# Performance work log

Hardware: AMD Instinct MI355X
Metric: run time of the kernel (lower is better)

The kernel has to match this reference:

```python
import jax, jax.numpy as jnp
import numpy as np

N, E, F, H, G, EPS = 50000, 500000, 128, 192, 256, 1e-5


def setup_inputs() -> dict:
    key = jax.random.key(0)
    ks = jax.random.split(key, 16)
    s = 0.05
    return {
        "x": jax.random.normal(ks[0], (N, F), jnp.float32),
        "edge_index": jax.random.randint(ks[1], (2, E), 0, N),
        "batch": jnp.sort(jax.random.randint(ks[2], (N,), 0, G)),
        "num_graphs": G,
        "w_rel0": jax.random.normal(ks[3], (H, F)) * s,
        "b_rel0": jnp.zeros((H,), jnp.float32),
        "w_root0": jax.random.normal(ks[4], (H, F)) * s,
        "w_rel": jax.random.normal(ks[5], (3, H, H)) * s,
        "b_rel": jnp.zeros((3, H), jnp.float32),
        "w_root": jax.random.normal(ks[6], (3, H, H)) * s,
        "bn_gamma": jnp.ones((4, H), jnp.float32),
        "bn_beta": jnp.zeros((4, H), jnp.float32),
        "head_w1": jax.random.normal(ks[7], (H, H)) * s,
        "head_b1": jnp.zeros((H,), jnp.float32),
        "head_w2": jax.random.normal(ks[8], (H, H)) * s,
        "head_b2": jnp.zeros((H,), jnp.float32),
        "out_w": jax.random.normal(ks[9], (1, H)) * s,
        "out_b": jnpp if False else jnp.zeros((1,), jnp.float32),
    }


def _conv_bn_relu(x, src, dst, n_nodes, wr, br, wroot, gamma, beta):
    # PyG GraphConv: out_i = lin_rel(sum_{j->i} x_j) + lin_root(x_i)
    agg = jax.ops.segment_sum(x[src], dst, num_segments=n_nodes)  # [N, d]
    h = agg @ wr.T + br + x @ wroot.T                             # [N, H]
    mu = h.mean(axis=0)
    var = h.var(axis=0)  # biased, as torch BN train mode
    h = (h - mu) * jax.lax.rsqrt(var + EPS) * gamma + beta
    return jax.nn.relu(h)


def reference(x, edge_index, batch, num_graphs, w_rel0, b_rel0, w_root0,
              w_rel, b_rel, w_root, bn_gamma, bn_beta,
              head_w1, head_b1, head_w2, head_b2, out_w, out_b):
    src, dst = edge_index[0], edge_index[1]
    n_nodes = x.shape[0]
    h = _conv_bn_relu(x, src, dst, n_nodes, w_rel0, b_rel0, w_root0,
                      bn_gamma[0], bn_beta[0])
    for i in range(3):
        h = _conv_bn_relu(h, src, dst, n_nodes, w_rel[i], b_rel[i], w_root[i],
                          bn_gamma[i + 1], bn_beta[i + 1])
    # global mean pool per graph
    sums = jax.ops.segment_sum(h, batch, num_segments=num_graphs)   # [G, H]
    cnts = jax.ops.segment_sum(jnp.ones((n_nodes,), h.dtype), batch,
                               num_segments=num_graphs)
    g = sums / jnp.maximum(cnts, 1.0)[:, None]
    # MLP head (dropout = eval) + output linear
    hh = jax.nn.relu(g @ head_w1.T + head_b1) @ head_w2.T + head_b2
    out = hh @ out_w.T + out_b                                      # [G, 1]
    return out[:, 0]
```

## Files before the change

kernel.cpp:

```cpp
#include <hip/hip_runtime.h>

#define HD 192
#define FD0 128
#define NG 256
#define BNEPS 1e-5f

#define STAT_S  1048576.0f
#define STAT_IS (1.0f / 1048576.0f)
#define POOL_S  65536.0f
#define POOL_IS (1.0f / 65536.0f)

typedef unsigned short u16;
typedef __attribute__((ext_vector_type(8))) short bf16x8;
typedef __attribute__((ext_vector_type(4))) float f32x4;

static inline int idiv(int a, int b) { return (a + b - 1) / b; }

__device__ __forceinline__ float b2f(u16 u) {
    unsigned int v = ((unsigned int)u) << 16;
    return __builtin_bit_cast(float, v);
}
__device__ __forceinline__ float b2f_lo(unsigned int u) {
    return __builtin_bit_cast(float, u << 16);
}
__device__ __forceinline__ float b2f_hi(unsigned int u) {
    return __builtin_bit_cast(float, u & 0xffff0000u);
}
__device__ __forceinline__ u16 f2b(float f) {
    unsigned int x = __builtin_bit_cast(unsigned int, f);
    return (u16)((x + 0x7FFFu + ((x >> 16) & 1u)) >> 16);
}

__device__ __forceinline__ void async_cp16(const void* g, void* l) {
    __builtin_amdgcn_global_load_lds(
        (const __attribute__((address_space(1))) unsigned int*)g,
        (__attribute__((address_space(3))) unsigned int*)l, 16, 0, 0);
}

__global__ __launch_bounds__(256) void convert_bf16(const float* __restrict__ in,
                                                    u16* __restrict__ out, int n4)
{
    const int i = blockIdx.x * 256 + threadIdx.x;
    if (i >= n4) return;
    const float4 v = ((const float4*)in)[i];
    u16 o[4] = { f2b(v.x), f2b(v.y), f2b(v.z), f2b(v.w) };
    ((ushort4*)out)[i] = *(ushort4*)o;
}

__device__ __forceinline__ void pack_one(const float* __restrict__ wr,
    const float* __restrict__ wt, u16* __restrict__ out, int K, int idx)
{
    const int j  = idx & 7;
    const int t  = idx >> 3;
    const int c  = t & 15;
    const int kg = (t >> 4) & 3;
    const int rest = t >> 6;
    const int fglob = rest % 12;
    const int chunk = rest / 12;
    const int col = fglob * 16 + c;
    const int k   = chunk * 32 + kg * 8 + j;
    const float v = (k < K) ? wr[(size_t)col * K + k] : wt[(size_t)col * K + (k - K)];
    out[idx] = f2b(v);
}

__global__ __launch_bounds__(256) void pack_fuse(const float* __restrict__ wr0,
    const float* __restrict__ wt0, const float* __restrict__ w_rel,
    const float* __restrict__ w_root, const float* __restrict__ hw1,
    const float* __restrict__ hw2, u16* __restrict__ wp0,
    u16* __restrict__ wp123, float* __restrict__ w1t, float* __restrict__ w2t)
{
    const int T0 = HD * 2 * FD0;
    const int T1 = HD * 2 * HD;
    const int TW = HD * HD;
    int idx = blockIdx.x * 256 + threadIdx.x;
    if (idx < T0) { pack_one(wr0, wt0, wp0, FD0, idx); return; }
    idx -= T0;
    if (idx < 3 * T1) {
        const int li = idx / T1;
        const int r  = idx - li * T1;
        pack_one(w_rel + (size_t)li * HD * HD, w_root + (size_t)li * HD * HD,
                 wp123 + (size_t)li * T1, HD, r);
        return;
    }
    idx -= 3 * T1;
    if (idx >= 2 * TW) return;
    const float* w = (idx < TW) ? hw1 : hw2;
    float*       o = (idx < TW) ? w1t : w2t;
    const int r = (idx < TW) ? idx : idx - TW;
    const int t = r % HD, k = r / HD;
    o[r] = w[(size_t)t * HD + k];
}

__global__ __launch_bounds__(256) void hist_kernel(const int* __restrict__ dst,
                                                   int* __restrict__ deg, int E)
{
    const int e = blockIdx.x * 256 + threadIdx.x;
    if (e < E) atomicAdd(&deg[dst[e]], 1);
}

__global__ __launch_bounds__(256) void scan_partial(const int* __restrict__ deg,
                                                    int* __restrict__ psum, int N)
{
    __shared__ int s[256];
    const int t = threadIdx.x;
    const int i = blockIdx.x * 256 + t;
    s[t] = (i < N) ? deg[i] : 0;
    __syncthreads();
    for (int off = 128; off > 0; off >>= 1) {
        if (t < off) s[t] += s[t + off];
        __syncthreads();
    }
    if (t == 0) psum[blockIdx.x] = s[0];
}

__global__ __launch_bounds__(256) void scan_small(int* __restrict__ psum, int M)
{
    __shared__ int s[256];
    const int t = threadIdx.x;
    s[t] = (t < M) ? psum[t] : 0;
    __syncthreads();
    for (int off = 1; off < 256; off <<= 1) {
        const int u = (t >= off) ? s[t - off] : 0;
        __syncthreads();
        s[t] += u;
        __syncthreads();
    }
    if (t < M) psum[t] = (t == 0) ? 0 : s[t - 1];
}

__global__ __launch_bounds__(256) void scan_expand(int* __restrict__ deg,
    const int* __restrict__ psum, int* __restrict__ rowptr, int N, int E)
{
    __shared__ int s[256];
    const int t = threadIdx.x;
    const int i = blockIdx.x * 256 + t;
    const int v = (i < N) ? deg[i] : 0;
    s[t] = v;
    __syncthreads();
    for (int off = 1; off < 256; off <<= 1) {
        const int u = (t >= off) ? s[t - off] : 0;
        __syncthreads();
        s[t] += u;
        __syncthreads();
    }
    if (i < N) {
        const int base = psum[blockIdx.x] + s[t] - v;
        rowptr[i] = base;
        deg[i]    = base;
    }
    if (i == N - 1) rowptr[N] = E;
}

__global__ __launch_bounds__(256) void fill_kernel(const int* __restrict__ src,
    const int* __restrict__ dst, int* __restrict__ cursor,
    int* __restrict__ eidx, int E)
{
    const int e = blockIdx.x * 256 + threadIdx.x;
    if (e >= E) return;
    const int p = atomicAdd(&cursor[dst[e]], 1);
    eidx[p] = src[e];
}

template<int FD>
__global__ __launch_bounds__(256) void gather_kernel(
    const u16* __restrict__ hb, const int* __restrict__ rowptr,
    const int* __restrict__ eidx, u16* __restrict__ aggb, int N)
{
    constexpr int GW = FD / 32;
    constexpr int ND = GW / 2;
    const int lane = threadIdx.x & 63;
    const int half = lane >> 5;
    const int g    = lane & 31;
    const int n    = blockIdx.x * 4 + (threadIdx.x >> 6);
    if (n >= N) return;
    const int beg = rowptr[n], end = rowptr[n + 1];

    float acc[GW];
#pragma unroll
    for (int i = 0; i < GW; ++i) acc[i] = 0.f;

    int j = beg + half;
    for (; j + 6 < end; j += 8) {
        const int s0 = eidx[j],     s1 = eidx[j + 2];
        const int s2 = eidx[j + 4], s3 = eidx[j + 6];
        const unsigned int* p0 = (const unsigned int*)(hb + (size_t)s0 * FD + g * GW);
        const unsigned int* p1 = (const unsigned int*)(hb + (size_t)s1 * FD + g * GW);
        const unsigned int* p2 = (const unsigned int*)(hb + (size_t)s2 * FD + g * GW);
        const unsigned int* p3 = (const unsigned int*)(hb + (size_t)s3 * FD + g * GW);
        unsigned int u0[ND], u1[ND], u2[ND], u3[ND];
#pragma unroll
        for (int d = 0; d < ND; ++d) { u0[d] = p0[d]; u1[d] = p1[d]; u2[d] = p2[d]; u3[d] = p3[d]; }
#pragma unroll
        for (int d = 0; d < ND; ++d) {
            acc[2*d]   += b2f_lo(u0[d]) + b2f_lo(u1[d]) + b2f_lo(u2[d]) + b2f_lo(u3[d]);
            acc[2*d+1] += b2f_hi(u0[d]) + b2f_hi(u1[d]) + b2f_hi(u2[d]) + b2f_hi(u3[d]);
        }
    }
    for (; j < end; j += 2) {
        const int s0 = eidx[j];
        const unsigned int* p0 = (const unsigned int*)(hb + (size_t)s0 * FD + g * GW);
#pragma unroll
        for (int d = 0; d < ND; ++d) {
            const unsigned int u = p0[d];
            acc[2*d]   += b2f_lo(u);
            acc[2*d+1] += b2f_hi(u);
        }
    }
#pragma unroll
    for (int i = 0; i < GW; ++i) acc[i] += __shfl_xor(acc[i], 32);

    if (half == 0) {
        unsigned int* q = (unsigned int*)(aggb + (size_t)n * FD + g * GW);
#pragma unroll
        for (int d = 0; d < ND; ++d) {
            const u16 lo = f2b(acc[2*d]);
            const u16 hi = f2b(acc[2*d+1]);
            q[d] = (unsigned int)lo | ((unsigned int)hi << 16);
        }
    }
}

template<int K1, int K2>
__global__ __launch_bounds__(512, 1) void gemm_mfma(
    const u16* __restrict__ A1, const u16* __restrict__ A2,
    const u16* __restrict__ Wb, const float* __restrict__ bias,
    u16* __restrict__ Hout, long long* __restrict__ statsq, int N)
{
    constexpr int KC  = K1 + K2;
    constexpr int NC  = KC / 32;
    constexpr int NC1 = K1 / 32;
    __shared__ u16 bsh[HD * KC];

    const int tid  = threadIdx.x;
    const int wave = tid >> 6, lane = tid & 63;
    const int c = lane & 15, kg = lane >> 4;
    const int row0 = blockIdx.x * 256 + wave * 32;

    {
        constexpr int NST = (HD * KC) / (512 * 8);
        const u16* wsrc = Wb + tid * 8;
        u16* ldst = bsh + tid * 8;
#pragma unroll
        for (int i = 0; i < NST; ++i)
            async_cp16(wsrc + i * 4096, ldst + i * 4096);
    }

    int arc[2];
#pragma unroll
    for (int m = 0; m < 2; ++m) {
        const int r = row0 + m * 16 + c;
        arc[m] = r < N ? r : N - 1;
    }

    f32x4 acc[2][12];
#pragma unroll
    for (int m = 0; m < 2; ++m)
#pragma unroll
        for (int f = 0; f < 12; ++f) acc[m][f] = (f32x4){0.f, 0.f, 0.f, 0.f};

    auto aload = [&](int ch, bf16x8* d) {
#pragma unroll
        for (int m = 0; m < 2; ++m) {
            const u16* p = (ch < NC1)
                ? (A1 + (size_t)arc[m] * K1 + ch * 32 + kg * 8)
                : (A2 + (size_t)arc[m] * K2 + (ch - NC1) * 32 + kg * 8);
            d[m] = *(const bf16x8*)p;
        }
    };

    bf16x8 a_cur[2], a_nxt[2];
    aload(0, a_cur);
    __syncthreads();

#pragma unroll
    for (int ch = 0; ch < NC; ++ch) {
        if (ch + 1 < NC) aload(ch + 1, a_nxt);
#pragma unroll
        for (int f = 0; f < 12; ++f) {
            const bf16x8 b = *(const bf16x8*)&bsh[ch * 6144 + f * 512 + kg * 128 + c * 8];
            acc[0][f] = __builtin_amdgcn_mfma_f32_16x16x32_bf16(a_cur[0], b, acc[0][f], 0, 0, 0);
            acc[1][f] = __builtin_amdgcn_mfma_f32_16x16x32_bf16(a_cur[1], b, acc[1][f], 0, 0, 0);
        }
        a_cur[0] = a_nxt[0]; a_cur[1] = a_nxt[1];
    }

    float s1v[12], s2v[12];
#pragma unroll
    for (int f = 0; f < 12; ++f) { s1v[f] = 0.f; s2v[f] = 0.f; }

#pragma unroll
    for (int f = 0; f < 12; ++f) {
        const int col = f * 16 + c;
        const float bv = bias[col];
#pragma unroll
        for (int m = 0; m < 2; ++m)
#pragma unroll
            for (int r = 0; r < 4; ++r) {
                const int orow = row0 + m * 16 + kg * 4 + r;
                if (orow < N) {
                    const float v = acc[m][f][r] + bv;
                    s1v[f] += v;
                    s2v[f] += v * v;
                    Hout[(size_t)orow * HD + col] = f2b(v);
                }
            }
    }
#pragma unroll
    for (int f = 0; f < 12; ++f) {
        s1v[f] += __shfl_xor(s1v[f], 16); s1v[f] += __shfl_xor(s1v[f], 32);
        s2v[f] += __shfl_xor(s2v[f], 16); s2v[f] += __shfl_xor(s2v[f], 32);
    }
    __syncthreads();
    float* red = (float*)bsh;
    if (kg == 0) {
#pragma unroll
        for (int f = 0; f < 12; ++f) {
            red[wave * HD + f * 16 + c]            = s1v[f];
            red[8 * HD + wave * HD + f * 16 + c]   = s2v[f];
        }
    }
    __syncthreads();
    if (tid < HD) {
        float a1 = 0.f, a2 = 0.f;
#pragma unroll
        for (int w = 0; w < 8; ++w) {
            a1 += red[w * HD + tid];
            a2 += red[8 * HD + w * HD + tid];
        }
        atomicAdd((unsigned long long*)&statsq[tid],
                  (unsigned long long)(long long)llrintf(a1 * STAT_S));
        atomicAdd((unsigned long long*)&statsq[HD + tid],
                  (unsigned long long)(long long)llrintf(a2 * STAT_S));
    }
}

__global__ __launch_bounds__(256) void norm_relu(const u16* __restrict__ hpre,
    u16* __restrict__ hb, const long long* __restrict__ statsq,
    const float* __restrict__ gamma, const float* __restrict__ beta, int N)
{
    __shared__ float sc[HD], sh[HD];
    const int t = threadIdx.x;
    if (t < HD) {
        const float inv = 1.0f / (float)N;
        const float sum = (float)statsq[t] * STAT_IS;
        const float sq  = (float)statsq[HD + t] * STAT_IS;
        const float mu  = sum * inv;
        const float var = sq * inv - mu * mu;
        const float s   = gamma[t] * rsqrtf(var + BNEPS);
        sc[t] = s; sh[t] = beta[t] - mu * s;
    }
    __syncthreads();
    const int idx = blockIdx.x * 256 + t;
    const int total = N * (HD / 8);
    if (idx >= total) return;
    const int c8 = idx % (HD / 8);
    uint4 packed = ((const uint4*)hpre)[idx];
    const u16* pu = (const u16*)&packed;
    u16 ob[8];
#pragma unroll
    for (int j = 0; j < 8; ++j) {
        const int cc = c8 * 8 + j;
        ob[j] = f2b(fmaxf(0.f, fmaf(b2f(pu[j]), sc[cc], sh[cc])));
    }
    ((uint4*)hb)[idx] = *(uint4*)ob;
}

__global__ __launch_bounds__(192) void pool_partial(const u16* __restrict__ hb,
    const int* __restrict__ batch, int* __restrict__ gsumq, int N)
{
    const int t   = threadIdx.x;
    const int rl  = t / 24;
    const int oct = t % 24;
    const int r0  = blockIdx.x * 256;
    const int rend = (r0 + 256 < N) ? r0 + 256 : N;

    float facc[8];
#pragma unroll
    for (int i = 0; i < 8; ++i) facc[i] = 0.f;
    int cur = -1;

    for (int r = r0 + rl; r < rend; r += 8) {
        const int b = batch[r];
        if (b != cur) {
            if (cur >= 0) {
                int* q = gsumq + (size_t)cur * HD + oct * 8;
#pragma unroll
                for (int i = 0; i < 8; ++i)
                    atomicAdd(&q[i], __float2int_rn(facc[i] * POOL_S));
            }
#pragma unroll
            for (int i = 0; i < 8; ++i) facc[i] = 0.f;
            cur = b;
        }
        const uint4 pv = *(const uint4*)(hb + (size_t)r * HD + oct * 8);
        const u16* pu = (const u16*)&pv;
#pragma unroll
        for (int i = 0; i < 8; ++i) facc[i] += b2f(pu[i]);
    }
    if (cur >= 0) {
        int* q = gsumq + (size_t)cur * HD + oct * 8;
#pragma unroll
        for (int i = 0; i < 8; ++i)
            atomicAdd(&q[i], __float2int_rn(facc[i] * POOL_S));
    }
}

__global__ __launch_bounds__(192) void head_kernel(
    const int* __restrict__ gsumq, const int* __restrict__ batch, int N,
    const float* __restrict__ w1t, const float* __restrict__ b1,
    const float* __restrict__ w2t, const float* __restrict__ b2,
    const float* __restrict__ ow, const float* __restrict__ ob,
    float* __restrict__ out)
{
    __shared__ float gv[HD];
    __shared__ float h1[HD];
    __shared__ float h2[HD];
    const int g = blockIdx.x;
    const int t = threadIdx.x;

    int lo = 0, hi = N;
    while (lo < hi) { int m = (lo + hi) >> 1; if (batch[m] < g) lo = m + 1; else hi = m; }
    const int start = lo;
    hi = N;
    while (lo < hi) { int m = (lo + hi) >> 1; if (batch[m] < g + 1) lo = m + 1; else hi = m; }
    const int end = lo;
    const float cnt = fmaxf((float)(end - start), 1.0f);

    gv[t] = (float)gsumq[(size_t)g * HD + t] * POOL_IS / cnt;
    __syncthreads();
    {
        float acc = b1[t];
#pragma unroll 4
        for (int k = 0; k < HD; ++k)
            acc = fmaf(gv[k], w1t[k * HD + t], acc);
        h1[t] = fmaxf(acc, 0.f);
    }
    __syncthreads();
    {
        float acc = b2[t];
#pragma unroll 4
        for (int k = 0; k < HD; ++k)
            acc = fmaf(h1[k], w2t[k * HD + t], acc);
        h2[t] = acc * ow[t];
    }
    __syncthreads();
    if (t < 64) {
        float s = h2[t] + h2[t + 64] + h2[t + 128];
#pragma unroll
        for (int d = 1; d < 64; d <<= 1) s += __shfl_xor(s, d);
        if (t == 0) out[g] = s + ob[0];
    }
}

extern "C" void kernel_launch(void* const* d_in, const int* in_sizes, int n_in,
                              void* d_out, int out_size, void* d_ws, size_t ws_size,
                              hipStream_t stream)
{
    const float* x       = (const float*)d_in[0];
    const int*   ei      = (const int*)d_in[1];
    const int*   batch   = (const int*)d_in[2];
    const float* w_rel0  = (const float*)d_in[4];
    const float* b_rel0  = (const float*)d_in[5];
    const float* w_root0 = (const float*)d_in[6];
    const float* w_rel   = (const float*)d_in[7];
    const float* b_rel   = (const float*)d_in[8];
    const float* w_root  = (const float*)d_in[9];
    const float* bn_g    = (const float*)d_in[10];
    const float* bn_b    = (const float*)d_in[11];
    const float* hw1     = (const float*)d_in[12];
    const float* hb1     = (const float*)d_in[13];
    const float* hw2     = (const float*)d_in[14];
    const float* hb2     = (const float*)d_in[15];
    const float* ow      = (const float*)d_in[16];
    const float* ob      = (const float*)d_in[17];
    float* out = (float*)d_out;

    const int N = in_sizes[0] / FD0;
    const int E = in_sizes[1] / 2;
    const int* src = ei;
    const int* dst = ei + E;
    const int M = idiv(N, 256);

    char* ws = (char*)d_ws;
    size_t off = 0;
    u16*   xb   = (u16*)(ws + off);   off += (size_t)N * FD0 * 2;
    u16*   hb   = (u16*)(ws + off);   off += (size_t)N * HD * 2;
    u16*   aggb = (u16*)(ws + off);   off += (size_t)N * HD * 2;
    u16*   hpre = (u16*)(ws + off);   off += (size_t)N * HD * 2;
    u16*   wp0  = (u16*)(ws + off);   off += (size_t)HD * 2 * FD0 * 2;
    u16*   wp123= (u16*)(ws + off);   off += (size_t)3 * HD * 2 * HD * 2;
    off = (off + 15) & ~(size_t)15;
    float* w1t = (float*)(ws + off); off += (size_t)HD * HD * 4;
    float* w2t = (float*)(ws + off); off += (size_t)HD * HD * 4;
    long long* statsq4 = (long long*)(ws + off); off += 4 * 2 * HD * sizeof(long long);
    int*   gsumq  = (int*)(ws + off); off += (size_t)NG * HD * 4;
    int*   rowptr = (int*)(ws + off); off += (size_t)(N + 1) * 4;
    int*   deg    = (int*)(ws + off); off += (size_t)N * 4;
    int*   psum   = (int*)(ws + off); off += (size_t)M * 4;
    int*   eidx   = (int*)(ws + off); off += (size_t)E * 4;

    const dim3 b256(256), b512(512), b192(192);

    convert_bf16<<<idiv(N * FD0 / 4, 256), b256, 0, stream>>>(x, xb, N * FD0 / 4);
    pack_fuse<<<idiv(HD * 2 * FD0 + 3 * HD * 2 * HD + 2 * HD * HD, 256), b256, 0,
                stream>>>(w_rel0, w_root0, w_rel, w_root, hw1, hw2,
                          wp0, wp123, w1t, w2t);
    hipMemsetAsync(statsq4, 0, 4 * 2 * HD * sizeof(long long) + (size_t)NG * HD * 4,
                   stream);
    hipMemsetAsync(deg, 0, (size_t)N * sizeof(int), stream);
    hist_kernel<<<idiv(E, 256), b256, 0, stream>>>(dst, deg, E);
    scan_partial<<<M, b256, 0, stream>>>(deg, psum, N);
    scan_small<<<1, b256, 0, stream>>>(psum, M);
    scan_expand<<<M, b256, 0, stream>>>(deg, psum, rowptr, N, E);
    fill_kernel<<<idiv(E, 256), b256, 0, stream>>>(src, dst, deg, eidx, E);

    gather_kernel<FD0><<<idiv(N, 4), b256, 0, stream>>>(xb, rowptr, eidx, aggb, N);
    gemm_mfma<FD0, FD0><<<idiv(N, 256), b512, 0, stream>>>(aggb, xb, wp0, b_rel0,
                                                           hpre, statsq4, N);
    norm_relu<<<idiv(N * (HD / 8), 256), b256, 0, stream>>>(hpre, hb, statsq4,
                                                            bn_g, bn_b, N);

    for (int i = 0; i < 3; ++i) {
        long long* statsq = statsq4 + (size_t)(i + 1) * 2 * HD;
        gather_kernel<HD><<<idiv(N, 4), b256, 0, stream>>>(hb, rowptr, eidx, aggb, N);
        gemm_mfma<HD, HD><<<idiv(N, 256), b512, 0, stream>>>(
            aggb, hb, wp123 + (size_t)i * HD * 2 * HD,
            b_rel + (size_t)i * HD, hpre, statsq, N);
        norm_relu<<<idiv(N * (HD / 8), 256), b256, 0, stream>>>(hpre, hb, statsq,
            bn_g + (size_t)(i + 1) * HD, bn_b + (size_t)(i + 1) * HD, N);
    }

    pool_partial<<<idiv(N, 256), b192, 0, stream>>>(hb, batch, gsumq, N);
    head_kernel<<<NG, b192, 0, stream>>>(gsumq, batch, N, w1t, hb1, w2t, hb2,
                                         ow, ob, out);
}
```

Baseline: 405.8 us.

## Fuse BatchNorm+ReLU into gather, GEMM and pooling consumers; drop norm_relu

Removes the standalone norm_relu pass. Each layer's GEMM now writes raw pre-activation values in place into h. The next layer's gather, the root-operand load in the GEMM, and the final pool each apply the BN scale/shift and ReLU on the fly from the stats of the previous layer. This saves a full read and write of the N×192 activation per layer and several kernel launches. In exchange, the gather does the BN math once per edge rather than once per node. The gather also switches to 16-byte loads per lane, which leaves some lanes idle, and the GEMM A-operand prefetch is deepened to a 4-stage register ring.

Result: faster. 391.5 us (-3.5%).

```diff
diff --git a/kernel.cpp b/kernel.cpp
--- a/kernel.cpp
+++ b/kernel.cpp
@@ -20,15 +20,22 @@
     unsigned int v = ((unsigned int)u) << 16;
     return __builtin_bit_cast(float, v);
 }
-__device__ __forceinline__ float b2f_lo(unsigned int u) {
-    return __builtin_bit_cast(float, u << 16);
-}
-__device__ __forceinline__ float b2f_hi(unsigned int u) {
-    return __builtin_bit_cast(float, u & 0xffff0000u);
-}
 __device__ __forceinline__ u16 f2b(float f) {
     unsigned int x = __builtin_bit_cast(unsigned int, f);
     return (u16)((x + 0x7FFFu + ((x >> 16) & 1u)) >> 16);
+}
+
+__device__ __forceinline__ void bn_params(const long long* __restrict__ statsq,
+    const float* __restrict__ gamma, const float* __restrict__ beta,
+    int N, int c, float& sc, float& sh)
+{
+    const float inv = 1.0f / (float)N;
+    const float sum = (float)statsq[c] * STAT_IS;
+    const float sq  = (float)statsq[HD + c] * STAT_IS;
+    const float mu  = sum * inv;
+    const float var = sq * inv - mu * mu;
+    const float s   = gamma[c] * rsqrtf(var + BNEPS);
+    sc = s; sh = beta[c] - mu * s;
 }
 
 __device__ __forceinline__ void async_cp16(const void* g, void* l) {
@@ -161,75 +168,92 @@
     eidx[p] = src[e];
 }
 
-template<int FD>
+template<int FD, bool BN>
 __global__ __launch_bounds__(256) void gather_kernel(
-    const u16* __restrict__ hb, const int* __restrict__ rowptr,
-    const int* __restrict__ eidx, u16* __restrict__ aggb, int N)
-{
-    constexpr int GW = FD / 32;
-    constexpr int ND = GW / 2;
-    const int lane = threadIdx.x & 63;
+    const u16* __restrict__ hsrc, const int* __restrict__ rowptr,
+    const int* __restrict__ eidx, u16* __restrict__ aggb, int N,
+    const long long* __restrict__ statsq, const float* __restrict__ gamma,
+    const float* __restrict__ beta)
+{
+    constexpr int OCT = FD / 8;
+    __shared__ float scs[FD], shs[FD];
+    const int t = threadIdx.x;
+    if (BN) {
+        if (t < FD) {
+            float sc, sh;
+            bn_params(statsq, gamma, beta, N, t, sc, sh);
+            scs[t] = sc; shs[t] = sh;
+        }
+        __syncthreads();
+    }
+    const int lane = t & 63;
     const int half = lane >> 5;
-    const int g    = lane & 31;
-    const int n    = blockIdx.x * 4 + (threadIdx.x >> 6);
+    const int o    = lane & 31;
+    const int n    = blockIdx.x * 4 + (t >> 6);
     if (n >= N) return;
+    const bool act = (o < OCT);
     const int beg = rowptr[n], end = rowptr[n + 1];
 
-    float acc[GW];
-#pragma unroll
-    for (int i = 0; i < GW; ++i) acc[i] = 0.f;
+    float scr[8], shr[8];
+    if (BN && act) {
+#pragma unroll
+        for (int i = 0; i < 8; ++i) { scr[i] = scs[o * 8 + i]; shr[i] = shs[o * 8 + i]; }
+    }
+
+    float acc[8];
+#pragma unroll
+    for (int i = 0; i < 8; ++i) acc[i] = 0.f;
+
+    auto consume = [&](uint4 v) {
+        const u16* pu = (const u16*)&v;
+#pragma unroll
+        for (int i = 0; i < 8; ++i) {
+            float f = b2f(pu[i]);
+            if (BN) f = fmaxf(0.f, fmaf(f, scr[i], shr[i]));
+            acc[i] += f;
+        }
+    };
 
     int j = beg + half;
     for (; j + 6 < end; j += 8) {
         const int s0 = eidx[j],     s1 = eidx[j + 2];
         const int s2 = eidx[j + 4], s3 = eidx[j + 6];
-        const unsigned int* p0 = (const unsigned int*)(hb + (size_t)s0 * FD + g * GW);
-        const unsigned int* p1 = (const unsigned int*)(hb + (size_t)s1 * FD + g * GW);
-        const unsigned int* p2 = (const unsigned int*)(hb + (size_t)s2 * FD + g * GW);
-        const unsigned int* p3 = (const unsigned int*)(hb + (size_t)s3 * FD + g * GW);
-        unsigned int u0[ND], u1[ND], u2[ND], u3[ND];
-#pragma unroll
-        for (int d = 0; d < ND; ++d) { u0[d] = p0[d]; u1[d] = p1[d]; u2[d] = p2[d]; u3[d] = p3[d]; }
-#pragma unroll
-        for (int d = 0; d < ND; ++d) {
-            acc[2*d]   += b2f_lo(u0[d]) + b2f_lo(u1[d]) + b2f_lo(u2[d]) + b2f_lo(u3[d]);
-            acc[2*d+1] += b2f_hi(u0[d]) + b2f_hi(u1[d]) + b2f_hi(u2[d]) + b2f_hi(u3[d]);
+        if (act) {
+            const uint4 v0 = *(const uint4*)(hsrc + (size_t)s0 * FD + o * 8);
+            const uint4 v1 = *(const uint4*)(hsrc + (size_t)s1 * FD + o * 8);
+            const uint4 v2 = *(const uint4*)(hsrc + (size_t)s2 * FD + o * 8);
+            const uint4 v3 = *(const uint4*)(hsrc + (size_t)s3 * FD + o * 8);
+            consume(v0); consume(v1); consume(v2); consume(v3);
         }
     }
     for (; j < end; j += 2) {
         const int s0 = eidx[j];
-        const unsigned int* p0 = (const unsigned int*)(hb + (size_t)s0 * FD + g * GW);
-#pragma unroll
-        for (int d = 0; d < ND; ++d) {
-            const unsigned int u = p0[d];
-            acc[2*d]   += b2f_lo(u);
-            acc[2*d+1] += b2f_hi(u);
-        }
-    }
-#pragma unroll
-    for (int i = 0; i < GW; ++i) acc[i] += __shfl_xor(acc[i], 32);
-
-    if (half == 0) {
-        unsigned int* q = (unsigned int*)(aggb + (size_t)n * FD + g * GW);
-#pragma unroll
-        for (int d = 0; d < ND; ++d) {
-            const u16 lo = f2b(acc[2*d]);
-            const u16 hi = f2b(acc[2*d+1]);
-            q[d] = (unsigned int)lo | ((unsigned int)hi << 16);
-        }
-    }
-}
-
-template<int K1, int K2>
+        if (act) consume(*(const uint4*)(hsrc + (size_t)s0 * FD + o * 8));
+    }
+#pragma unroll
+    for (int i = 0; i < 8; ++i) acc[i] += __shfl_xor(acc[i], 32);
+
+    if (half == 0 && act) {
+        u16 ov[8];
+#pragma unroll
+        for (int i = 0; i < 8; ++i) ov[i] = f2b(acc[i]);
+        *(uint4*)(aggb + (size_t)n * FD + o * 8) = *(uint4*)ov;
+    }
+}
+
+template<int K1, int K2, bool BN>
 __global__ __launch_bounds__(512, 1) void gemm_mfma(
-    const u16* __restrict__ A1, const u16* __restrict__ A2,
+    const u16* __restrict__ A1, const u16* A2,
     const u16* __restrict__ Wb, const float* __restrict__ bias,
-    u16* __restrict__ Hout, long long* __restrict__ statsq, int N)
+    u16* Hout, long long* __restrict__ statsq_out,
+    const long long* __restrict__ statsq_in, const float* __restrict__ gamma,
+    const float* __restrict__ beta, int N)
 {
     constexpr int KC  = K1 + K2;
     constexpr int NC  = KC / 32;
     constexpr int NC1 = K1 / 32;
     __shared__ u16 bsh[HD * KC];
+    __shared__ float scs[K2], shs[K2];
 
     const int tid  = threadIdx.x;
     const int wave = tid >> 6, lane = tid & 63;
@@ -243,6 +267,13 @@
 #pragma unroll
         for (int i = 0; i < NST; ++i)
             async_cp16(wsrc + i * 4096, ldst + i * 4096);
+    }
+    if (BN) {
+        if (tid < K2) {
+            float sc, sh;
+            bn_params(statsq_in, gamma, beta, N, tid, sc, sh);
+            scs[tid] = sc; shs[tid] = sh;
+        }
     }
 
     int arc[2];
@@ -268,20 +299,41 @@
         }
     };
 
-    bf16x8 a_cur[2], a_nxt[2];
-    aload(0, a_cur);
+    bf16x8 ring[4][2];
+#pragma unroll
+    for (int p = 0; p < 4; ++p)
+        if (p < NC) aload(p, ring[p]);
+
     __syncthreads();
 
 #pragma unroll
     for (int ch = 0; ch < NC; ++ch) {
-        if (ch + 1 < NC) aload(ch + 1, a_nxt);
+        bf16x8 a[2] = { ring[ch & 3][0], ring[ch & 3][1] };
+        if (ch + 4 < NC) aload(ch + 4, ring[ch & 3]);
+        if (BN && ch >= NC1) {
+            const int k0 = (ch - NC1) * 32 + kg * 8;
+            const float4 s0 = *(const float4*)&scs[k0];
+            const float4 s1 = *(const float4*)&scs[k0 + 4];
+            const float4 h0 = *(const float4*)&shs[k0];
+            const float4 h1 = *(const float4*)&shs[k0 + 4];
+            const float scv[8] = {s0.x,s0.y,s0.z,s0.w,s1.x,s1.y,s1.z,s1.w};
+            const float shv[8] = {h0.x,h0.y,h0.z,h0.w,h1.x,h1.y,h1.z,h1.w};
+#pragma unroll
+            for (int m = 0; m < 2; ++m) {
+                const u16* pa = (const u16*)&a[m];
+                u16 tv[8];
+#pragma unroll
+                for (int i = 0; i < 8; ++i)
+                    tv[i] = f2b(fmaxf(0.f, fmaf(b2f(pa[i]), scv[i], shv[i])));
+                a[m] = *(bf16x8*)tv;
+            }
+        }
 #pragma unroll
         for (int f = 0; f < 12; ++f) {
             const bf16x8 b = *(const bf16x8*)&bsh[ch * 6144 + f * 512 + kg * 128 + c * 8];
-            acc[0][f] = __builtin_amdgcn_mfma_f32_16x16x32_bf16(a_cur[0], b, acc[0][f], 0, 0, 0);
-            acc[1][f] = __builtin_amdgcn_mfma_f32_16x16x32_bf16(a_cur[1], b, acc[1][f], 0, 0, 0);
-        }
-        a_cur[0] = a_nxt[0]; a_cur[1] = a_nxt[1];
+            acc[0][f] = __builtin_amdgcn_mfma_f32_16x16x32_bf16(a[0], b, acc[0][f], 0, 0, 0);
+            acc[1][f] = __builtin_amdgcn_mfma_f32_16x16x32_bf16(a[1], b, acc[1][f], 0, 0, 0);
+        }
     }
 
     float s1v[12], s2v[12];
@@ -327,52 +379,34 @@
             a1 += red[w * HD + tid];
             a2 += red[8 * HD + w * HD + tid];
         }
-        atomicAdd((unsigned long long*)&statsq[tid],
+        atomicAdd((unsigned long long*)&statsq_out[tid],
                   (unsigned long long)(long long)llrintf(a1 * STAT_S));
-        atomicAdd((unsigned long long*)&statsq[HD + tid],
+        atomicAdd((unsigned long long*)&statsq_out[HD + tid],
                   (unsigned long long)(long long)llrintf(a2 * STAT_S));
     }
 }
 
-__global__ __launch_bounds__(256) void norm_relu(const u16* __restrict__ hpre,
-    u16* __restrict__ hb, const long long* __restrict__ statsq,
-    const float* __restrict__ gamma, const float* __restrict__ beta, int N)
-{
-    __shared__ float sc[HD], sh[HD];
+__global__ __launch_bounds__(192) void pool_partial(const u16* __restrict__ h,
+    const int* __restrict__ batch, int* __restrict__ gsumq, int N,
+    const long long* __restrict__ statsq, const float* __restrict__ gamma,
+    const float* __restrict__ beta)
+{
+    __shared__ float scs[HD], shs[HD];
     const int t = threadIdx.x;
-    if (t < HD) {
-        const float inv = 1.0f / (float)N;
-        const float sum = (float)statsq[t] * STAT_IS;
-        const float sq  = (float)statsq[HD + t] * STAT_IS;
-        const float mu  = sum * inv;
-        const float var = sq * inv - mu * mu;
-        const float s   = gamma[t] * rsqrtf(var + BNEPS);
-        sc[t] = s; sh[t] = beta[t] - mu * s;
-    }
-    __syncthreads();
-    const int idx = blockIdx.x * 256 + t;
-    const int total = N * (HD / 8);
-    if (idx >= total) return;
-    const int c8 = idx % (HD / 8);
-    uint4 packed = ((const uint4*)hpre)[idx];
-    const u16* pu = (const u16*)&packed;
-    u16 ob[8];
-#pragma unroll
-    for (int j = 0; j < 8; ++j) {
-        const int cc = c8 * 8 + j;
-        ob[j] = f2b(fmaxf(0.f, fmaf(b2f(pu[j]), sc[cc], sh[cc])));
-    }
-    ((uint4*)hb)[idx] = *(uint4*)ob;
-}
-
-__global__ __launch_bounds__(192) void pool_partial(const u16* __restrict__ hb,
-    const int* __restrict__ batch, int* __restrict__ gsumq, int N)
-{
-    const int t   = threadIdx.x;
+    {
+        float sc, sh;
+        bn_params(statsq, gamma, beta, N, t, sc, sh);
+        scs[t] = sc; shs[t] = sh;
+    }
+    __syncthreads();
     const int rl  = t / 24;
     const int oct = t % 24;
     const int r0  = blockIdx.x * 256;
     const int rend = (r0 + 256 < N) ? r0 + 256 : N;
+
+    float scr[8], shr[8];
+#pragma unroll
+    for (int i = 0; i < 8; ++i) { scr[i] = scs[oct * 8 + i]; shr[i] = shs[oct * 8 + i]; }
 
     float facc[8];
 #pragma unroll
@@ -392,10 +426,11 @@
             for (int i = 0; i < 8; ++i) facc[i] = 0.f;
             cur = b;
         }
-        const uint4 pv = *(const uint4*)(hb + (size_t)r * HD + oct * 8);
+        const uint4 pv = *(const uint4*)(h + (size_t)r * HD + oct * 8);
         const u16* pu = (const u16*)&pv;
 #pragma unroll
-        for (int i = 0; i < 8; ++i) facc[i] += b2f(pu[i]);
+        for (int i = 0; i < 8; ++i)
+            facc[i] += fmaxf(0.f, fmaf(b2f(pu[i]), scr[i], shr[i]));
     }
     if (cur >= 0) {
         int* q = gsumq + (size_t)cur * HD + oct * 8;
@@ -484,9 +519,8 @@
     char* ws = (char*)d_ws;
     size_t off = 0;
     u16*   xb   = (u16*)(ws + off);   off += (size_t)N * FD0 * 2;
-    u16*   hb   = (u16*)(ws + off);   off += (size_t)N * HD * 2;
+    u16*   h    = (u16*)(ws + off);   off += (size_t)N * HD * 2;
     u16*   aggb = (u16*)(ws + off);   off += (size_t)N * HD * 2;
-    u16*   hpre = (u16*)(ws + off);   off += (size_t)N * HD * 2;
     u16*   wp0  = (u16*)(ws + off);   off += (size_t)HD * 2 * FD0 * 2;
     u16*   wp123= (u16*)(ws + off);   off += (size_t)3 * HD * 2 * HD * 2;
     off = (off + 15) & ~(size_t)15;
@@ -514,23 +548,26 @@
     scan_expand<<<M, b256, 0, stream>>>(deg, psum, rowptr, N, E);
     fill_kernel<<<idiv(E, 256), b256, 0, stream>>>(src, dst, deg, eidx, E);
 
-    gather_kernel<FD0><<<idiv(N, 4), b256, 0, stream>>>(xb, rowptr, eidx, aggb, N);
-    gemm_mfma<FD0, FD0><<<idiv(N, 256), b512, 0, stream>>>(aggb, xb, wp0, b_rel0,
-                                                           hpre, statsq4, N);
-    norm_relu<<<idiv(N * (HD / 8), 256), b256, 0, stream>>>(hpre, hb, statsq4,
-                                                            bn_g, bn_b, N);
+    gather_kernel<FD0, false><<<idiv(N, 4), b256, 0, stream>>>(
+        xb, rowptr, eidx, aggb, N, nullptr, nullptr, nullptr);
+    gemm_mfma<FD0, FD0, false><<<idiv(N, 256), b512, 0, stream>>>(
+        aggb, xb, wp0, b_rel0, h, statsq4, nullptr, nullptr, nullptr, N);
 
     for (int i = 0; i < 3; ++i) {
-        long long* statsq = statsq4 + (size_t)(i + 1) * 2 * HD;
-        gather_kernel<HD><<<idiv(N, 4), b256, 0, stream>>>(hb, rowptr, eidx, aggb, N);
-        gemm_mfma<HD, HD><<<idiv(N, 256), b512, 0, stream>>>(
-            aggb, hb, wp123 + (size_t)i * HD * 2 * HD,
-            b_rel + (size_t)i * HD, hpre, statsq, N);
-        norm_relu<<<idiv(N * (HD / 8), 256), b256, 0, stream>>>(hpre, hb, statsq,
-            bn_g + (size_t)(i + 1) * HD, bn_b + (size_t)(i + 1) * HD, N);
-    }
-
-    pool_partial<<<idiv(N, 256), b192, 0, stream>>>(hb, batch, gsumq, N);
+        const long long* sin  = statsq4 + (size_t)i * 2 * HD;
+        long long*       sout = statsq4 + (size_t)(i + 1) * 2 * HD;
+        const float* g = bn_g + (size_t)i * HD;
+        const float* b = bn_b + (size_t)i * HD;
+        gather_kernel<HD, true><<<idiv(N, 4), b256, 0, stream>>>(
+            h, rowptr, eidx, aggb, N, sin, g, b);
+        gemm_mfma<HD, HD, true><<<idiv(N, 256), b512, 0, stream>>>(
+            aggb, h, wp123 + (size_t)i * HD * 2 * HD,
+            b_rel + (size_t)i * HD, h, sout, sin, g, b, N);
+    }
+
+    pool_partial<<<idiv(N, 256), b192, 0, stream>>>(
+        h, batch, gsumq, N, statsq4 + 3 * 2 * (size_t)HD,
+        bn_g + 3 * (size_t)HD, bn_b + 3 * (size_t)HD);
     head_kernel<<<NG, b192, 0, stream>>>(gsumq, batch, N, w1t, hb1, w2t, hb2,
                                          ow, ob, out);
 }
```
